# Optimization experiments

Hardware: AMD Instinct MI355X
Metric: run time of the kernel (lower is better)

The kernel has to match this reference:

```python
import jax, jax.numpy as jnp
import numpy as np

B, S, D = 2, 1024, 1024
NH, DQK, DH = 8, 64, 128
CAP = 15.0
EPS = 1e-6


def setup_inputs() -> dict:
    key = jax.random.key(0)
    ks = jax.random.split(key, 8)
    s = 0.02
    return {
        "x": jax.random.normal(ks[0], (B, S, D), jnp.float32),
        "Wq": jax.random.normal(ks[1], (D, NH * DQK), jnp.float32) * s,
        "Wk": jax.random.normal(ks[2], (D, NH * DQK), jnp.float32) * s,
        "Wv": jax.random.normal(ks[3], (D, NH * DH), jnp.float32) * s,
        "Wi": jax.random.normal(ks[4], (D, NH), jnp.float32) * s,
        "bi": jnp.zeros((NH,), jnp.float32),
        "Wf": jax.random.normal(ks[5], (D, NH), jnp.float32) * s,
        "bf": jnp.ones((NH,), jnp.float32),
        "Wog": jax.random.normal(ks[6], (D, D), jnp.float32) * s,
        "ln_w": jnp.ones((NH, DH), jnp.float32),
        "ln_b": jnp.zeros((NH, DH), jnp.float32),
        "Wout": jax.random.normal(ks[7], (NH * DH, D), jnp.float32) * s,
    }


def _mlstm_scan(q, k, v, i, f):
    # q,k: [S,B,NH,DQK]; v: [S,B,NH,DH]; i,f: [S,B,NH]
    b, nh, dqk, dh = q.shape[1], q.shape[2], q.shape[3], v.shape[3]
    scale = dqk ** -0.5
    c0 = jnp.zeros((b, nh, dqk, dh), jnp.float32)
    m0 = jnp.zeros((b, nh), jnp.float32)

    def step(carry, inp):
        c, m = carry
        qt, kt, vt, it, ft = inp
        flog = jax.nn.log_sigmoid(ft)
        m_new = jnp.maximum(flog + m, it)
        f_act = jnp.exp(flog + m - m_new)
        i_act = jnp.exp(it - m_new)
        kv = jnp.einsum('bhi,bhj->bhij', kt, vt)
        c_new = f_act[..., None, None] * c + i_act[..., None, None] * kv
        ht = jnp.einsum('bhij,bhi->bhj', c_new, qt * scale)
        return (c_new, m_new), ht

    _, h = jax.lax.scan(step, (c0, m0), (q, k, v, i, f))
    return h  # [S,B,NH,DH]


def reference(x, Wq, Wk, Wv, Wi, bi, Wf, bf, Wog, ln_w, ln_b, Wout):
    b, s, d = x.shape
    nh, dh = ln_w.shape
    dqk = Wq.shape[1] // nh
    # projections -> time-major [S,B,NH,*]
    q = (x @ Wq).reshape(b, s, nh, dqk).transpose(1, 0, 2, 3)
    k = (x @ Wk).reshape(b, s, nh, dqk).transpose(1, 0, 2, 3)
    v = (x @ Wv).reshape(b, s, nh, dh).transpose(1, 0, 2, 3)
    i = (x @ Wi + bi).transpose(1, 0, 2)
    f = (x @ Wf + bf).transpose(1, 0, 2)
    h = _mlstm_scan(q, k, v, i, f)           # [S,B,NH,DH]
    h = h.transpose(1, 2, 0, 3)              # [B,NH,S,DH]
    # per-head layernorm (unbiased=False variance)
    mean = h.mean(-1, keepdims=True)
    var = ((h - mean) ** 2).mean(-1, keepdims=True)
    hn = (h - mean) / jnp.sqrt(var + EPS)
    hn = hn * ln_w[None, :, None, :] + ln_b[None, :, None, :]
    hn = hn.transpose(0, 2, 1, 3).reshape(b, s, nh * dh)  # [B,S,v_dim]
    o = jax.nn.sigmoid(jnp.tanh((x @ Wog) / CAP) * CAP)
    return (hn * o) @ Wout
```

## Files before the change

### kernel.cpp

```cpp
#include <hip/hip_runtime.h>
#include <math.h>

#define NB_B   2
#define NB_S   1024
#define NB_D   1024
#define NB_NH  8
#define NB_DQK 64
#define NB_DH  128
#define NCH    8
#define CL     128

typedef __attribute__((ext_vector_type(8))) short  short8v;
typedef __attribute__((ext_vector_type(4))) float  f32x4;
typedef __attribute__((ext_vector_type(8))) unsigned short ushort8v;
typedef __attribute__((ext_vector_type(4))) unsigned short ushort4v;

__device__ __forceinline__ unsigned short f2bf(float f) {
  unsigned u = __float_as_uint(f);
  unsigned r = (u + 0x7FFFu + ((u >> 16) & 1u)) >> 16;
  return (unsigned short)r;
}
__device__ __forceinline__ float bf2f(unsigned short h) {
  return __uint_as_float(((unsigned)h) << 16);
}

#define GLD_LDS16(g, l) __builtin_amdgcn_global_load_lds( \
    (const __attribute__((address_space(1))) void*)(g),   \
    (__attribute__((address_space(3))) void*)(l), 16, 0, 0)

#define MFMA_BF16(a, b, c) __builtin_amdgcn_mfma_f32_16x16x32_bf16((a), (b), (c), 0, 0, 0)

constexpr size_t BF(size_t elems) { return elems / 2; }
constexpr size_t SZ_QK1 = BF(2048ull * 512);
constexpr size_t SZ_PVX = BF(2048ull * 2048);
constexpr size_t SZ_XH  = BF(2048ull * 1024);
constexpr size_t SZ_XL  = BF(2048ull * 1024);
constexpr size_t SZ_WHI = BF(3072ull * 1024);
constexpr size_t SZ_WLO = BF(1024ull * 1024);
constexpr size_t SZ_WTO = BF(1024ull * 1024);
constexpr size_t SZ_GBUF= 16ull * 1024;
constexpr size_t SZ_DL  = 16ull * 8 * 8192;
constexpr size_t SZ_HNG = BF(2048ull * 1024);

constexpr size_t OFF_QH  = 0;
constexpr size_t OFF_QL  = OFF_QH  + SZ_QK1;
constexpr size_t OFF_KH  = OFF_QL  + SZ_QK1;
constexpr size_t OFF_KL  = OFF_KH  + SZ_QK1;
constexpr size_t OFF_PVX = OFF_KL  + SZ_QK1;
constexpr size_t OFF_XH  = OFF_PVX + SZ_PVX;
constexpr size_t OFF_XL  = OFF_XH  + SZ_XH;
constexpr size_t OFF_WHI = OFF_XL  + SZ_XL;
constexpr size_t OFF_WLO = OFF_WHI + SZ_WHI;
constexpr size_t OFF_WTO = OFF_WLO + SZ_WLO;
constexpr size_t OFF_IV  = OFF_WTO + SZ_WTO;
constexpr size_t OFF_FV  = OFF_IV  + SZ_GBUF;
constexpr size_t OFF_G   = OFF_FV  + SZ_GBUF;
constexpr size_t OFF_GM  = OFF_G   + SZ_GBUF;
constexpr size_t OFF_DL  = OFF_GM  + SZ_GBUF;
constexpr size_t OFF_HNG = OFF_DL  + SZ_DL;
constexpr size_t WS_TOTAL = OFF_HNG + SZ_HNG;
static_assert(OFF_PVX == 2097152, "Qh+Ql+Kh+Kl must equal old Pqk footprint");
static_assert(SZ_QK1 == 524288, "each qk plane is 2048x512 bf16 = 524,288 float slots");

__device__ __forceinline__ void transp_body(
    const float* __restrict__ src,
    unsigned short* __restrict__ hi, unsigned short* __restrict__ lo,
    int N, int nt, int kt, int tid, float (*Ls)[65])
{
  #pragma unroll
  for (int p = 0; p < 16; ++p) {
    int lin = p * 256 + tid;
    int kr = lin >> 6, nc = lin & 63;
    Ls[kr][nc] = src[(size_t)(kt*64 + kr) * N + nt*64 + nc];
  }
  __syncthreads();
  #pragma unroll
  for (int p = 0; p < 16; ++p) {
    int lin = p * 256 + tid;
    int nr = lin >> 6, kc = lin & 63;
    float v = Ls[kc][nr];
    unsigned short h = f2bf(v);
    size_t di = (size_t)(nt*64 + nr) * 1024 + kt*64 + kc;
    hi[di] = h;
    if (lo) lo[di] = f2bf(v - bf2f(h));
  }
}

__global__ __launch_bounds__(256) void prep(
    const float* __restrict__ x,
    const float* __restrict__ Wi, const float* __restrict__ bi,
    const float* __restrict__ Wf, const float* __restrict__ bf,
    const float* __restrict__ Wq, const float* __restrict__ Wk,
    const float* __restrict__ Wv, const float* __restrict__ Wog,
    const float* __restrict__ Wout,
    unsigned short* __restrict__ xh, unsigned short* __restrict__ xl,
    float* __restrict__ iv, float* __restrict__ fv,
    unsigned short* __restrict__ Whi, unsigned short* __restrict__ Wlo,
    unsigned short* __restrict__ WtO)
{
  __shared__ float Ls[64][65];
  const int bx = blockIdx.x, tid = threadIdx.x;
  if (bx < 512) {
    const int row = bx * 4 + (tid >> 6);
    const int l = tid & 63;
    const float4* xr4 = (const float4*)(x + (size_t)row * NB_D);
    float ai[8] = {}, af[8] = {};
    #pragma unroll
    for (int p = 0; p < 4; ++p) {
      int q4i = l + p * 64;
      float4 xv = xr4[q4i];
      int k0 = q4i * 4;
      const float* xs = (const float*)&xv;
      ushort4v h4, l4;
      #pragma unroll
      for (int j = 0; j < 4; ++j) {
        float xsv = xs[j];
        unsigned short hh = f2bf(xsv);
        h4[j] = hh; l4[j] = f2bf(xsv - bf2f(hh));
        const float4* wi4 = (const float4*)(Wi + (size_t)(k0 + j) * 8);
        const float4* wf4 = (const float4*)(Wf + (size_t)(k0 + j) * 8);
        float4 w0 = wi4[0], w1 = wi4[1];
        float4 v0 = wf4[0], v1 = wf4[1];
        ai[0] += xsv*w0.x; ai[1] += xsv*w0.y; ai[2] += xsv*w0.z; ai[3] += xsv*w0.w;
        ai[4] += xsv*w1.x; ai[5] += xsv*w1.y; ai[6] += xsv*w1.z; ai[7] += xsv*w1.w;
        af[0] += xsv*v0.x; af[1] += xsv*v0.y; af[2] += xsv*v0.z; af[3] += xsv*v0.w;
        af[4] += xsv*v1.x; af[5] += xsv*v1.y; af[6] += xsv*v1.z; af[7] += xsv*v1.w;
      }
      *(ushort4v*)(xh + (size_t)row * NB_D + k0) = h4;
      *(ushort4v*)(xl + (size_t)row * NB_D + k0) = l4;
    }
    #pragma unroll
    for (int off = 1; off < 64; off <<= 1) {
      #pragma unroll
      for (int cc = 0; cc < 8; ++cc) {
        ai[cc] += __shfl_xor(ai[cc], off);
        af[cc] += __shfl_xor(af[cc], off);
      }
    }
    if (l == 0) {
      int b = row >> 10, s = row & (NB_S - 1);
      #pragma unroll
      for (int cc = 0; cc < 8; ++cc) {
        iv[(size_t)(b*NB_NH + cc) * NB_S + s] = ai[cc] + bi[cc];
        fv[(size_t)(b*NB_NH + cc) * NB_S + s] = af[cc] + bf[cc];
      }
    }
  } else {
    const int idx = bx - 512;
    const int xq = idx & 63, kt = idx >> 6;
    if (xq < 8)       transp_body(Wq,   Whi,              Wlo,            512,  xq,      kt, tid, Ls);
    else if (xq < 16) transp_body(Wk,   Whi +  512*1024,  Wlo + 512*1024, 512,  xq - 8,  kt, tid, Ls);
    else if (xq < 32) transp_body(Wv,   Whi + 1024*1024,  nullptr,        1024, xq - 16, kt, tid, Ls);
    else if (xq < 48) transp_body(Wog,  Whi + 2048*1024,  nullptr,        1024, xq - 32, kt, tid, Ls);
    else              transp_body(Wout, WtO,              nullptr,        1024, xq - 48, kt, tid, Ls);
  }
}

__global__ __launch_bounds__(256) void gemm_proj(
    const unsigned short* __restrict__ xh,
    const unsigned short* __restrict__ xl,
    const unsigned short* __restrict__ Whi,
    const unsigned short* __restrict__ Wlo,
    unsigned short* __restrict__ Qh, unsigned short* __restrict__ Ql,
    unsigned short* __restrict__ Kh, unsigned short* __restrict__ Kl,
    unsigned short* __restrict__ Pvx,
    const float* __restrict__ iv, const float* __restrict__ fv,
    float* __restrict__ gv, float* __restrict__ Gv)
{
  __shared__ __align__(16) char smem[49152];
  const int tid  = threadIdx.x;

  if (blockIdx.x < 16) {
    if (tid >= 64) return;
    const int bh = blockIdx.x, l = tid;
    const int base = bh * NB_S + l * 16;
    float fl[16];
    float run = 0.f;
    #pragma unroll
    for (int u = 0; u < 16; ++u) {
      float fr = fv[base + u];
      float flog = (fr >= 0.f) ? -log1pf(expf(-fr)) : (fr - log1pf(expf(fr)));
      run += flog; fl[u] = run;
    }
    float tot = run, sc = tot;
    #pragma unroll
    for (int off = 1; off < 64; off <<= 1) {
      float t = __shfl_up(sc, off);
      if (l >= off) sc += t;
    }
    float excl = sc - tot;
    float gm[16]; float rmax = -1e30f;
    #pragma unroll
    for (int u = 0; u < 16; ++u) {
      float bt = excl + fl[u];
      float g = iv[base + u] - bt;
      gv[base + u] = g;
      rmax = fmaxf(rmax, g); gm[u] = rmax;
    }
    float mx = rmax;
    #pragma unroll
    for (int off = 1; off < 64; off <<= 1) {
      float t = __shfl_up(mx, off);
      if (l >= off) mx = fmaxf(mx, t);
    }
    float em = __shfl_up(mx, 1);
    if (l == 0) em = -1e30f;
    #pragma unroll
    for (int u = 0; u < 16; ++u)
      Gv[base + u] = fmaxf(0.f, fmaxf(em, gm[u]));
    return;
  }

  const int gx   = blockIdx.x - 16;
  const int bid  = ((gx & 7) << 6) | (gx >> 3);
  const int wid  = tid >> 6, lane = tid & 63;
  const int wm   = wid >> 1, wn = wid & 1;
  const int lrow = lane & 15;
  const int lk   = (lane >> 4) * 16;
  const int srow = tid >> 3;
  const int scb  = (tid & 7) << 4;
  const int ldsW = wid * 1024;

  if (!(bid & 1)) {
    const int h  = bid >> 1;
    const int ct = h & 7, bm = h >> 3;
    char* Ah = smem;
    char* Al = smem + 8192;
    char* Bh = smem + 16384;
    char* Bl = smem + 32768;
    const char* xhB = (const char*)xh;
    const char* xlB = (const char*)xl;
    const char* whB = (const char*)(Whi + (size_t)ct*128*1024);
    const char* wlB = (const char*)(Wlo + (size_t)ct*128*1024);

    size_t gA[2], gB[4];
    #pragma unroll
    for (int i = 0; i < 2; ++i) {
      int row = i * 32 + srow;
      int cbs = scb ^ ((row & 7) << 4);
      gA[i] = (size_t)(bm*64 + row) * 2048 + cbs;
    }
    #pragma unroll
    for (int i = 0; i < 4; ++i) {
      int row = i * 32 + srow;
      int cbs = scb ^ ((row & 7) << 4);
      gB[i] = (size_t)row * 2048 + cbs;
    }

    f32x4 acc[2][4];
    const f32x4 z4 = { 0.f, 0.f, 0.f, 0.f };
    #pragma unroll
    for (int m = 0; m < 2; ++m)
      #pragma unroll
      for (int n = 0; n < 4; ++n) acc[m][n] = z4;

    for (int kt = 0; kt < 16; ++kt) {
      __syncthreads();
      #pragma unroll
      for (int i = 0; i < 2; ++i) GLD_LDS16(xhB + gA[i] + kt*128, Ah + i*4096 + ldsW);
      #pragma unroll
      for (int i = 0; i < 2; ++i) GLD_LDS16(xlB + gA[i] + kt*128, Al + i*4096 + ldsW);
      #pragma unroll
      for (int i = 0; i < 4; ++i) GLD_LDS16(whB + gB[i] + kt*128, Bh + i*4096 + ldsW);
      #pragma unroll
      for (int i = 0; i < 4; ++i) GLD_LDS16(wlB + gB[i] + kt*128, Bl + i*4096 + ldsW);
      __syncthreads();

      #pragma unroll
      for (int kk = 0; kk < 2; ++kk) {
        short8v ah[2], al[2], bh[4], bl[4];
        #pragma unroll
        for (int m = 0; m < 2; ++m) {
          int row = wm*32 + m*16 + lrow;
          int kb  = (kk*64 + lk) ^ ((row & 7) << 4);
          ah[m] = *(const short8v*)(Ah + row*128 + kb);
          al[m] = *(const short8v*)(Al + row*128 + kb);
        }
        #pragma unroll
        for (int n = 0; n < 4; ++n) {
          int row = wn*64 + n*16 + lrow;
          int kb  = (kk*64 + lk) ^ ((row & 7) << 4);
          bh[n] = *(const short8v*)(Bh + row*128 + kb);
          bl[n] = *(const short8v*)(Bl + row*128 + kb);
        }
        #pragma unroll
        for (int m = 0; m < 2; ++m)
          #pragma unroll
          for (int n = 0; n < 4; ++n) {
            acc[m][n] = MFMA_BF16(ah[m], bh[n], acc[m][n]);
            acc[m][n] = MFMA_BF16(al[m], bh[n], acc[m][n]);
            acc[m][n] = MFMA_BF16(ah[m], bl[n], acc[m][n]);
          }
      }
    }

    const int crow0 = bm*64 + wm*32 + ((lane >> 4) << 2);
    const int ccol0 = (ct & 3)*128 + wn*64 + lrow;
    unsigned short* Hd = (ct < 4) ? Qh : Kh;
    unsigned short* Ld = (ct < 4) ? Ql : Kl;
    #pragma unroll
    for (int m = 0; m < 2; ++m)
      #pragma unroll
      for (int n = 0; n < 4; ++n)
        #pragma unroll
        for (int r = 0; r < 4; ++r) {
          float v = acc[m][n][r];
          unsigned short hh = f2bf(v);
          size_t idx = (size_t)(crow0 + m*16 + r) * 512 + ccol0 + n*16;
          Hd[idx] = hh;
          Ld[idx] = f2bf(v - bf2f(hh));
        }
  } else {
    const int l  = bid >> 1;
    const int ct = l & 15, bm = l >> 4;
    char* As = smem;
    char* Bs = smem + 16384;
    const char* xhB = (const char*)xh;
    const char* wB  = (const char*)(Whi + (size_t)(8 + ct)*128*1024);

    size_t gA[4], gB[4];
    #pragma unroll
    for (int i = 0; i < 4; ++i) {
      int row = i * 32 + srow;
      int cbs = scb ^ ((row & 7) << 4);
      gA[i] = (size_t)(bm*128 + row) * 2048 + cbs;
      gB[i] = (size_t)row * 2048 + cbs;
    }

    f32x4 acc[4][4];
    const f32x4 z4 = { 0.f, 0.f, 0.f, 0.f };
    #pragma unroll
    for (int m = 0; m < 4; ++m)
      #pragma unroll
      for (int n = 0; n < 4; ++n) acc[m][n] = z4;

    for (int kt = 0; kt < 16; ++kt) {
      __syncthreads();
      #pragma unroll
      for (int i = 0; i < 4; ++i) GLD_LDS16(xhB + gA[i] + kt*128, As + i*4096 + ldsW);
      #pragma unroll
      for (int i = 0; i < 4; ++i) GLD_LDS16(wB  + gB[i] + kt*128, Bs + i*4096 + ldsW);
      __syncthreads();

      #pragma unroll
      for (int kk = 0; kk < 2; ++kk) {
        short8v a[4], b[4];
        #pragma unroll
        for (int m = 0; m < 4; ++m) {
          int row = wm*64 + m*16 + lrow;
          int kb  = (kk*64 + lk) ^ ((row & 7) << 4);
          a[m] = *(const short8v*)(As + row*128 + kb);
        }
        #pragma unroll
        for (int n = 0; n < 4; ++n) {
          int row = wn*64 + n*16 + lrow;
          int kb  = (kk*64 + lk) ^ ((row & 7) << 4);
          b[n] = *(const short8v*)(Bs + row*128 + kb);
        }
        #pragma unroll
        for (int m = 0; m < 4; ++m)
          #pragma unroll
          for (int n = 0; n < 4; ++n)
            acc[m][n] = MFMA_BF16(a[m], b[n], acc[m][n]);
      }
    }

    const int crow0 = bm*128 + wm*64 + ((lane >> 4) << 2);
    const int ccol0 = ct*128 + wn*64 + lrow;
    #pragma unroll
    for (int m = 0; m < 4; ++m)
      #pragma unroll
      for (int n = 0; n < 4; ++n)
        #pragma unroll
        for (int r = 0; r < 4; ++r)
          Pvx[(size_t)(crow0 + m*16 + r) * 2048 + ccol0 + n*16] = f2bf(acc[m][n][r]);
  }
}

__global__ __launch_bounds__(256) void gemm_out64(
    const unsigned short* __restrict__ A,
    const unsigned short* __restrict__ Bt,
    float* __restrict__ C, int ldc)
{
  __shared__ __align__(16) unsigned short As[128*64];
  __shared__ __align__(16) unsigned short Bs[64*64];
  const int tid  = threadIdx.x;
  const int bid  = ((blockIdx.x & 7) << 5) | (blockIdx.x >> 3);
  const int cn   = bid & 15, bm = bid >> 4;
  const int wid  = tid >> 6, lane = tid & 63;
  const int wm   = wid >> 1, wn = wid & 1;
  const int lrow = lane & 15;
  const int lk   = (lane >> 4) * 16;

  f32x4 acc[4][2];
  const f32x4 z4 = { 0.f, 0.f, 0.f, 0.f };
  #pragma unroll
  for (int m = 0; m < 4; ++m)
    #pragma unroll
    for (int n = 0; n < 2; ++n) acc[m][n] = z4;

  const int srow = tid >> 3;
  const int scb  = (tid & 7) << 4;
  const char* Ab = (const char*)A;
  const char* Bb = (const char*)Bt;
  size_t gA[4], gB[2];
  #pragma unroll
  for (int i = 0; i < 4; ++i) {
    int row = i * 32 + srow;
    int cbs = scb ^ ((row & 7) << 4);
    gA[i] = (size_t)(bm*128 + row) * 2048 + cbs;
  }
  #pragma unroll
  for (int i = 0; i < 2; ++i) {
    int row = i * 32 + srow;
    int cbs = scb ^ ((row & 7) << 4);
    gB[i] = (size_t)(cn*64 + row) * 2048 + cbs;
  }
  const int ldsW = wid * 1024;

  for (int kt = 0; kt < 16; ++kt) {
    __syncthreads();
    #pragma unroll
    for (int i = 0; i < 4; ++i)
      GLD_LDS16(Ab + gA[i] + kt*128, (char*)As + i*4096 + ldsW);
    #pragma unroll
    for (int i = 0; i < 2; ++i)
      GLD_LDS16(Bb + gB[i] + kt*128, (char*)Bs + i*4096 + ldsW);
    __syncthreads();

    #pragma unroll
    for (int kk = 0; kk < 2; ++kk) {
      short8v a[4], b[2];
      #pragma unroll
      for (int m = 0; m < 4; ++m) {
        int row = wm*64 + m*16 + lrow;
        int kb  = (kk*64 + lk) ^ ((row & 7) << 4);
        a[m] = *(const short8v*)((const char*)As + row*128 + kb);
      }
      #pragma unroll
      for (int n = 0; n < 2; ++n) {
        int row = wn*32 + n*16 + lrow;
        int kb  = (kk*64 + lk) ^ ((row & 7) << 4);
        b[n] = *(const short8v*)((const char*)Bs + row*128 + kb);
      }
      #pragma unroll
      for (int m = 0; m < 4; ++m)
        #pragma unroll
        for (int n = 0; n < 2; ++n)
          acc[m][n] = MFMA_BF16(a[m], b[n], acc[m][n]);
    }
  }

  const int crow0 = bm*128 + wm*64 + ((lane >> 4) << 2);
  const int ccol0 = cn*64 + wn*32 + (lane & 15);
  #pragma unroll
  for (int m = 0; m < 4; ++m)
    #pragma unroll
    for (int n = 0; n < 2; ++n)
      #pragma unroll
      for (int r = 0; r < 4; ++r)
        C[(size_t)(crow0 + m*16 + r) * ldc + ccol0 + n*16] = acc[m][n][r];
}

__global__ __launch_bounds__(128) void chunk_local(
    const unsigned short* __restrict__ Kh, const unsigned short* __restrict__ Pvx,
    const float* __restrict__ gv, const float* __restrict__ Gv,
    float* __restrict__ Dloc)
{
  __shared__ float ks[16][68];
  __shared__ float vs[16][68];
  __shared__ float wsg[16];
  const int bx = ((blockIdx.x & 7) << 5) | (blockIdx.x >> 3);
  const int bh = bx >> 4, c = (bx >> 1) & 7, jh = bx & 1;
  const int b = bh >> 3, h = bh & 7;
  const int tid = threadIdx.x;
  const int rg = tid >> 3, cg = tid & 7;
  const int i0 = rg * 4;
  float acc[4][8] = {};
  const float Gend = Gv[bh*NB_S + c*CL + CL - 1];
  const unsigned short* kbp = Kh + ((size_t)b*NB_S + c*CL) * 512 + h*NB_DQK;
  const unsigned short* vbp = Pvx + ((size_t)b*NB_S + c*CL) * 2048 + h*NB_DH + jh*64;
  const float* gbp = gv + bh*NB_S + c*CL;
  for (int sb = 0; sb < 8; ++sb) {
    __syncthreads();
    #pragma unroll
    for (int p = 0; p < 2; ++p) {
      int qd = tid + p*128; int r = qd >> 4, cq = qd & 15;
      ushort4v k4 = *(const ushort4v*)(kbp + (size_t)(sb*16 + r)*512 + cq*4);
      ks[r][cq*4+0] = bf2f(k4[0]); ks[r][cq*4+1] = bf2f(k4[1]);
      ks[r][cq*4+2] = bf2f(k4[2]); ks[r][cq*4+3] = bf2f(k4[3]);
    }
    #pragma unroll
    for (int p = 0; p < 2; ++p) {
      int qd = tid + p*128; int r = qd >> 4, cq = qd & 15;
      ushort4v v4 = *(const ushort4v*)(vbp + (size_t)(sb*16 + r)*2048 + cq*4);
      vs[r][cq*4+0] = bf2f(v4[0]); vs[r][cq*4+1] = bf2f(v4[1]);
      vs[r][cq*4+2] = bf2f(v4[2]); vs[r][cq*4+3] = bf2f(v4[3]);
    }
    if (tid < 16) wsg[tid] = expf(gbp[sb*16 + tid] - Gend);
    __syncthreads();
    #pragma unroll
    for (int s = 0; s < 16; ++s) {
      float w = wsg[s];
      float4 kq = *(const float4*)(&ks[s][i0]);
      float wk[4] = { w*kq.x, w*kq.y, w*kq.z, w*kq.w };
      #pragma unroll
      for (int m = 0; m < 2; ++m) {
        float4 vq = *(const float4*)(&vs[s][cg*4 + m*32]);
        #pragma unroll
        for (int u = 0; u < 4; ++u) {
          acc[u][m*4+0] += wk[u]*vq.x;
          acc[u][m*4+1] += wk[u]*vq.y;
          acc[u][m*4+2] += wk[u]*vq.z;
          acc[u][m*4+3] += wk[u]*vq.w;
        }
      }
    }
  }
  float* dst = Dloc + ((size_t)bh*NCH + c) * (NB_DQK*NB_DH) + jh*64;
  #pragma unroll
  for (int u = 0; u < 4; ++u)
    #pragma unroll
    for (int m = 0; m < 2; ++m) {
      float4 o4 = { acc[u][m*4+0], acc[u][m*4+1], acc[u][m*4+2], acc[u][m*4+3] };
      *(float4*)(dst + (size_t)(i0+u)*NB_DH + cg*4 + m*32) = o4;
    }
}

__global__ __launch_bounds__(256,1) void chunk_out(
    const unsigned short* __restrict__ Qh, const unsigned short* __restrict__ Ql,
    const unsigned short* __restrict__ Kh, const unsigned short* __restrict__ Kl,
    const unsigned short* __restrict__ Pvx,
    const float* __restrict__ gv, const float* __restrict__ Gv,
    const float* __restrict__ Dloc,
    const float* __restrict__ lnw, const float* __restrict__ lnb,
    unsigned short* __restrict__ hng)
{
  __shared__ __align__(16) char smem[131072];
  __shared__ float gsh[128], Gsh[128], rsh[128];
  constexpr int QHo = 0, QLo = 8192, KHo = 16384, KLo = 32768;
  constexpr int ATT = 49152, VT = 65536, CBH = 98304, CBL = 114688;

  const int bx = ((blockIdx.x & 7) << 5) | (blockIdx.x >> 3);
  const int half = bx & 1, c = (bx >> 1) & 7, bh = bx >> 4;
  const int b = bh >> 3, h = bh & 7;
  const int tid = threadIdx.x;
  const int wid = tid >> 6, lane = tid & 63;
  const int lrow = lane & 15;
  const int lkB  = (lane >> 4) * 16;
  const size_t rowbase = (size_t)b*NB_S + (size_t)c*CL;
  const int sgbase = bh*NB_S + c*CL;
  const int ldsW = wid * 1024;

  {
    const int srow8 = tid >> 3;
    const int scb8  = (tid & 7) << 4;
    const char* QhB = (const char*)Qh;
    const char* QlB = (const char*)Ql;
    const char* KhB = (const char*)Kh;
    const char* KlB = (const char*)Kl;
    #pragma unroll
    for (int i = 0; i < 2; ++i) {
      int r = i*32 + srow8;
      size_t off = (size_t)(rowbase + half*64 + r)*1024 + h*128 + (scb8 ^ ((r & 7) << 4));
      GLD_LDS16(QhB + off, smem + QHo + i*4096 + ldsW);
      GLD_LDS16(QlB + off, smem + QLo + i*4096 + ldsW);
    }
    #pragma unroll
    for (int i = 0; i < 4; ++i) {
      int r = i*32 + srow8;
      size_t off = (size_t)(rowbase + r)*1024 + h*128 + (scb8 ^ ((r & 7) << 4));
      GLD_LDS16(KhB + off, smem + KHo + i*4096 + ldsW);
      GLD_LDS16(KlB + off, smem + KLo + i*4096 + ldsW);
    }
  }

  if (tid < 128) {
    float gval = gv[sgbase + tid];
    float Gval = Gv[sgbase + tid];
    gsh[tid] = gval; Gsh[tid] = Gval;
    float Gprev = (c > 0) ? Gv[sgbase - 1] : 0.f;
    rsh[tid] = 0.125f * expf(Gprev - Gval);
  }

  #pragma unroll
  for (int p = 0; p < 8; ++p) {
    int lin = p*256 + tid;
    int s = lin >> 4, j0 = (lin & 15) * 8;
    ushort8v v8 = *(const ushort8v*)(Pvx + (rowbase + s)*2048 + h*NB_DH + j0);
    #pragma unroll
    for (int j = 0; j < 8; ++j) {
      int jj = j0 + j;
      int off = (jj*256 + s*2) ^ ((jj & 7) << 4);
      *(unsigned short*)(smem + VT + off) = v8[j];
    }
  }
  {
    float4 cbacc[8];
    #pragma unroll
    for (int p = 0; p < 8; ++p) cbacc[p] = float4{0.f,0.f,0.f,0.f};
    const float Gcm1 = (c > 0) ? Gv[sgbase - 1] : 0.f;
    for (int cp = 0; cp < c; ++cp) {
      float wgt = expf(Gv[bh*NB_S + cp*CL + CL - 1] - Gcm1);
      const float4* dl4 = (const float4*)(Dloc + ((size_t)bh*NCH + cp)*8192);
      #pragma unroll
      for (int p = 0; p < 8; ++p) {
        float4 d = dl4[p*256 + tid];
        cbacc[p].x += wgt*d.x; cbacc[p].y += wgt*d.y;
        cbacc[p].z += wgt*d.z; cbacc[p].w += wgt*d.w;
      }
    }
    #pragma unroll
    for (int p = 0; p < 8; ++p) {
      int lin = p*256 + tid;
      int i = lin >> 5, j0 = (lin & 31) * 4;
      float vv[4] = { cbacc[p].x, cbacc[p].y, cbacc[p].z, cbacc[p].w };
      #pragma unroll
      for (int w = 0; w < 4; ++w) {
        int jj = j0 + w;
        int off = (jj*128 + i*2) ^ ((jj & 7) << 4);
        unsigned short hh = f2bf(vv[w]);
        *(unsigned short*)(smem + CBH + off) = hh;
        *(unsigned short*)(smem + CBL + off) = f2bf(vv[w] - bf2f(hh));
      }
    }
  }
  __syncthreads();

  const f32x4 z4 = { 0.f, 0.f, 0.f, 0.f };
  const int trow = wid*16 + lrow;

  f32x4 sacc[8];
  #pragma unroll
  for (int n = 0; n < 8; ++n) sacc[n] = z4;
  #pragma unroll
  for (int kk = 0; kk < 2; ++kk) {
    int qb = kk*64 + lkB;
    int ab = (trow*128 + qb) ^ ((trow & 7) << 4);
    short8v aqh = *(const short8v*)(smem + QHo + ab);
    short8v aql = *(const short8v*)(smem + QLo + ab);
    #pragma unroll
    for (int n = 0; n < 8; ++n) {
      int srw = n*16 + lrow;
      int bb = (srw*128 + qb) ^ ((srw & 7) << 4);
      short8v bkh = *(const short8v*)(smem + KHo + bb);
      short8v bkl = *(const short8v*)(smem + KLo + bb);
      sacc[n] = MFMA_BF16(aqh, bkh, sacc[n]);
      sacc[n] = MFMA_BF16(aql, bkh, sacc[n]);
      sacc[n] = MFMA_BF16(aqh, bkl, sacc[n]);
    }
  }
  {
    int td[4]; float gt[4];
    #pragma unroll
    for (int r = 0; r < 4; ++r) {
      td[r] = wid*16 + ((lane >> 4) << 2) + r;
      gt[r] = Gsh[half*64 + td[r]];
    }
    #pragma unroll
    for (int n = 0; n < 8; ++n) {
      int s = n*16 + lrow;
      float gs = gsh[s];
      #pragma unroll
      for (int r = 0; r < 4; ++r) {
        float w = 0.125f * expf(gs - gt[r]);
        float val = (s <= half*64 + td[r]) ? sacc[n][r]*w : 0.f;
        int off = (td[r]*256 + s*2) ^ ((td[r] & 7) << 4);
        *(unsigned short*)(smem + ATT + off) = f2bf(val);
      }
    }
  }

  f32x4 h2[8];
  #pragma unroll
  for (int n = 0; n < 8; ++n) h2[n] = z4;
  #pragma unroll
  for (int kk = 0; kk < 2; ++kk) {
    int qb = kk*64 + lkB;
    int ab = (trow*128 + qb) ^ ((trow & 7) << 4);
    short8v aqh = *(const short8v*)(smem + QHo + ab);
    short8v aql = *(const short8v*)(smem + QLo + ab);
    #pragma unroll
    for (int n = 0; n < 8; ++n) {
      int jrw = n*16 + lrow;
      int bb = (jrw*128 + qb) ^ ((jrw & 7) << 4);
      short8v bch = *(const short8v*)(smem + CBH + bb);
      short8v bcl = *(const short8v*)(smem + CBL + bb);
      h2[n] = MFMA_BF16(aqh, bch, h2[n]);
      h2[n] = MFMA_BF16(aql, bch, h2[n]);
      h2[n] = MFMA_BF16(aqh, bcl, h2[n]);
    }
  }
  __syncthreads();

  f32x4 h1[8];
  #pragma unroll
  for (int n = 0; n < 8; ++n) h1[n] = z4;
  #pragma unroll
  for (int kk = 0; kk < 4; ++kk) {
    int ab = (trow*256 + kk*64 + lkB) ^ ((trow & 7) << 4);
    short8v aat = *(const short8v*)(smem + ATT + ab);
    #pragma unroll
    for (int n = 0; n < 8; ++n) {
      int jrw = n*16 + lrow;
      int bb = (jrw*256 + kk*64 + lkB) ^ ((jrw & 7) << 4);
      short8v bvt = *(const short8v*)(smem + VT + bb);
      h1[n] = MFMA_BF16(aat, bvt, h1[n]);
    }
  }
  __syncthreads();

  float* Hb = (float*)smem;
  {
    #pragma unroll
    for (int r = 0; r < 4; ++r) {
      int tl = wid*16 + ((lane >> 4) << 2) + r;
      float rr = rsh[half*64 + tl];
      #pragma unroll
      for (int n = 0; n < 8; ++n)
        Hb[tl*132 + n*16 + lrow] = h1[n][r] + rr*h2[n][r];
    }
  }
  __syncthreads();

  const int tr = tid >> 4, tc = tid & 15;
  float lw[8], lb[8];
  {
    float4 a0 = *(const float4*)(lnw + h*NB_DH + tc*4);
    float4 a1 = *(const float4*)(lnw + h*NB_DH + tc*4 + 64);
    lw[0]=a0.x; lw[1]=a0.y; lw[2]=a0.z; lw[3]=a0.w;
    lw[4]=a1.x; lw[5]=a1.y; lw[6]=a1.z; lw[7]=a1.w;
    float4 b0 = *(const float4*)(lnb + h*NB_DH + tc*4);
    float4 b1 = *(const float4*)(lnb + h*NB_DH + tc*4 + 64);
    lb[0]=b0.x; lb[1]=b0.y; lb[2]=b0.z; lb[3]=b0.w;
    lb[4]=b1.x; lb[5]=b1.y; lb[6]=b1.z; lb[7]=b1.w;
  }
  #pragma unroll
  for (int u = 0; u < 4; ++u) {
    int tl = tr*4 + u;
    int t  = half*64 + tl;
    float hrow[8];
    float4 hl0 = *(const float4*)(&Hb[tl*132 + tc*4]);
    float4 hl1 = *(const float4*)(&Hb[tl*132 + tc*4 + 64]);
    hrow[0]=hl0.x; hrow[1]=hl0.y; hrow[2]=hl0.z; hrow[3]=hl0.w;
    hrow[4]=hl1.x; hrow[5]=hl1.y; hrow[6]=hl1.z; hrow[7]=hl1.w;
    float sum = 0.f, ssq = 0.f;
    #pragma unroll
    for (int x = 0; x < 8; ++x) { sum += hrow[x]; ssq += hrow[x]*hrow[x]; }
    #pragma unroll
    for (int off = 1; off < 16; off <<= 1) {
      sum += __shfl_xor(sum, off);
      ssq += __shfl_xor(ssq, off);
    }
    float mean = sum * (1.f/NB_DH);
    float var  = ssq * (1.f/NB_DH) - mean*mean;
    float rstd = rsqrtf(var + 1e-6f);
    #pragma unroll
    for (int m = 0; m < 2; ++m) {
      ushort4v xo4 = *(const ushort4v*)(Pvx + (rowbase + t)*2048 + 1024 + h*NB_DH + tc*4 + m*64);
      float xov[4] = { bf2f(xo4[0]), bf2f(xo4[1]), bf2f(xo4[2]), bf2f(xo4[3]) };
      unsigned short res[4];
      #pragma unroll
      for (int w = 0; w < 4; ++w) {
        int x = m*4 + w;
        float hn = (hrow[x] - mean)*rstd*lw[x] + lb[x];
        float tt = tanhf(xov[w]*(1.f/15.f))*15.f;
        float o = 1.f/(1.f + expf(-tt));
        res[w] = f2bf(hn*o);
      }
      ushort4v r4 = { res[0], res[1], res[2], res[3] };
      *(ushort4v*)(hng + (rowbase + t)*1024 + h*NB_DH + tc*4 + m*64) = r4;
    }
  }
}

extern "C" void kernel_launch(void* const* d_in, const int* in_sizes, int n_in,
                              void* d_out, int out_size, void* d_ws, size_t ws_size,
                              hipStream_t stream)
{
  (void)in_sizes; (void)n_in; (void)out_size; (void)ws_size;
  const float* x   = (const float*)d_in[0];
  const float* Wq  = (const float*)d_in[1];
  const float* Wk  = (const float*)d_in[2];
  const float* Wv  = (const float*)d_in[3];
  const float* Wi  = (const float*)d_in[4];
  const float* bi  = (const float*)d_in[5];
  const float* Wf  = (const float*)d_in[6];
  const float* bf  = (const float*)d_in[7];
  const float* Wog = (const float*)d_in[8];
  const float* lnw = (const float*)d_in[9];
  const float* lnb = (const float*)d_in[10];
  const float* Wout= (const float*)d_in[11];
  float* out = (float*)d_out;
  float* ws  = (float*)d_ws;

  unsigned short* Qh  = (unsigned short*)(ws + OFF_QH);
  unsigned short* Ql  = (unsigned short*)(ws + OFF_QL);
  unsigned short* Kh  = (unsigned short*)(ws + OFF_KH);
  unsigned short* Kl  = (unsigned short*)(ws + OFF_KL);
  unsigned short* Pvx = (unsigned short*)(ws + OFF_PVX);
  unsigned short* xh  = (unsigned short*)(ws + OFF_XH);
  unsigned short* xl  = (unsigned short*)(ws + OFF_XL);
  unsigned short* Whi = (unsigned short*)(ws + OFF_WHI);
  unsigned short* Wlo = (unsigned short*)(ws + OFF_WLO);
  unsigned short* WtO = (unsigned short*)(ws + OFF_WTO);
  float*          iv  = ws + OFF_IV;
  float*          fv  = ws + OFF_FV;
  float*          g   = ws + OFF_G;
  float*          G   = ws + OFF_GM;
  float*          Dl  = ws + OFF_DL;
  unsigned short* hng = (unsigned short*)(ws + OFF_HNG);

  prep     <<<1536, 256, 0, stream>>>(x, Wi, bi, Wf, bf, Wq, Wk, Wv, Wog, Wout,
                                      xh, xl, iv, fv, Whi, Wlo, WtO);

  gemm_proj<<<528, 256, 0, stream>>>(xh, xl, Whi, Wlo, Qh, Ql, Kh, Kl, Pvx,
                                     iv, fv, g, G);

  chunk_local<<<256, 128, 0, stream>>>(Kh, Pvx, g, G, Dl);
  chunk_out  <<<256, 256, 0, stream>>>(Qh, Ql, Kh, Kl, Pvx, g, G, Dl, lnw, lnb, hng);

  gemm_out64 <<<256, 256, 0, stream>>>(hng, WtO, out, 1024);
}
```

Before: 109.0 us.

## Fuse chunk_local and chunk_out into one cooperative kernel with grid sync

The per-chunk KV state computation now runs as the first phase of the chunk output kernel, using 256 threads per block and the existing shared memory. A grid-wide cooperative sync separates it from the output phase, and the kernel is launched with hipLaunchCooperativeKernel. The aim is to drop one kernel launch and its inter-kernel gap. In exchange it adds a grid barrier and requires all 256 blocks to be co-resident, which launch_bounds(256,1) and the 128KB+ shared memory allow on a 256-CU device.

```diff
diff --git a/kernel.cpp b/kernel.cpp
--- a/kernel.cpp
+++ b/kernel.cpp
@@ -1,5 +1,8 @@
 #include <hip/hip_runtime.h>
+#include <hip/hip_cooperative_groups.h>
 #include <math.h>
+
+namespace cg = cooperative_groups;
 
 #define NB_B   2
 #define NB_S   1024
@@ -462,77 +465,12 @@
         C[(size_t)(crow0 + m*16 + r) * ldc + ccol0 + n*16] = acc[m][n][r];
 }
 
-__global__ __launch_bounds__(128) void chunk_local(
-    const unsigned short* __restrict__ Kh, const unsigned short* __restrict__ Pvx,
-    const float* __restrict__ gv, const float* __restrict__ Gv,
-    float* __restrict__ Dloc)
-{
-  __shared__ float ks[16][68];
-  __shared__ float vs[16][68];
-  __shared__ float wsg[16];
-  const int bx = ((blockIdx.x & 7) << 5) | (blockIdx.x >> 3);
-  const int bh = bx >> 4, c = (bx >> 1) & 7, jh = bx & 1;
-  const int b = bh >> 3, h = bh & 7;
-  const int tid = threadIdx.x;
-  const int rg = tid >> 3, cg = tid & 7;
-  const int i0 = rg * 4;
-  float acc[4][8] = {};
-  const float Gend = Gv[bh*NB_S + c*CL + CL - 1];
-  const unsigned short* kbp = Kh + ((size_t)b*NB_S + c*CL) * 512 + h*NB_DQK;
-  const unsigned short* vbp = Pvx + ((size_t)b*NB_S + c*CL) * 2048 + h*NB_DH + jh*64;
-  const float* gbp = gv + bh*NB_S + c*CL;
-  for (int sb = 0; sb < 8; ++sb) {
-    __syncthreads();
-    #pragma unroll
-    for (int p = 0; p < 2; ++p) {
-      int qd = tid + p*128; int r = qd >> 4, cq = qd & 15;
-      ushort4v k4 = *(const ushort4v*)(kbp + (size_t)(sb*16 + r)*512 + cq*4);
-      ks[r][cq*4+0] = bf2f(k4[0]); ks[r][cq*4+1] = bf2f(k4[1]);
-      ks[r][cq*4+2] = bf2f(k4[2]); ks[r][cq*4+3] = bf2f(k4[3]);
-    }
-    #pragma unroll
-    for (int p = 0; p < 2; ++p) {
-      int qd = tid + p*128; int r = qd >> 4, cq = qd & 15;
-      ushort4v v4 = *(const ushort4v*)(vbp + (size_t)(sb*16 + r)*2048 + cq*4);
-      vs[r][cq*4+0] = bf2f(v4[0]); vs[r][cq*4+1] = bf2f(v4[1]);
-      vs[r][cq*4+2] = bf2f(v4[2]); vs[r][cq*4+3] = bf2f(v4[3]);
-    }
-    if (tid < 16) wsg[tid] = expf(gbp[sb*16 + tid] - Gend);
-    __syncthreads();
-    #pragma unroll
-    for (int s = 0; s < 16; ++s) {
-      float w = wsg[s];
-      float4 kq = *(const float4*)(&ks[s][i0]);
-      float wk[4] = { w*kq.x, w*kq.y, w*kq.z, w*kq.w };
-      #pragma unroll
-      for (int m = 0; m < 2; ++m) {
-        float4 vq = *(const float4*)(&vs[s][cg*4 + m*32]);
-        #pragma unroll
-        for (int u = 0; u < 4; ++u) {
-          acc[u][m*4+0] += wk[u]*vq.x;
-          acc[u][m*4+1] += wk[u]*vq.y;
-          acc[u][m*4+2] += wk[u]*vq.z;
-          acc[u][m*4+3] += wk[u]*vq.w;
-        }
-      }
-    }
-  }
-  float* dst = Dloc + ((size_t)bh*NCH + c) * (NB_DQK*NB_DH) + jh*64;
-  #pragma unroll
-  for (int u = 0; u < 4; ++u)
-    #pragma unroll
-    for (int m = 0; m < 2; ++m) {
-      float4 o4 = { acc[u][m*4+0], acc[u][m*4+1], acc[u][m*4+2], acc[u][m*4+3] };
-      *(float4*)(dst + (size_t)(i0+u)*NB_DH + cg*4 + m*32) = o4;
-    }
-}
-
-__global__ __launch_bounds__(256,1) void chunk_out(
+__global__ __launch_bounds__(256,1) void tail_fused(
     const unsigned short* __restrict__ Qh, const unsigned short* __restrict__ Ql,
     const unsigned short* __restrict__ Kh, const unsigned short* __restrict__ Kl,
     const unsigned short* __restrict__ Pvx,
     const float* __restrict__ gv, const float* __restrict__ Gv,
-    const float* __restrict__ Dloc,
+    float* __restrict__ Dloc,
     const float* __restrict__ lnw, const float* __restrict__ lnb,
     unsigned short* __restrict__ hng)
 {
@@ -541,10 +479,62 @@
   constexpr int QHo = 0, QLo = 8192, KHo = 16384, KLo = 32768;
   constexpr int ATT = 49152, VT = 65536, CBH = 98304, CBL = 114688;
 
+  const int tid = threadIdx.x;
   const int bx = ((blockIdx.x & 7) << 5) | (blockIdx.x >> 3);
+
+  {
+    const int bhA = bx >> 4, cA = (bx >> 1) & 7, jh = bx & 1;
+    const int bA = bhA >> 3, hA = bhA & 7;
+    float* ks = (float*)smem;
+    float* vs = (float*)(smem + 8192);
+    float* wsg = (float*)(smem + 16384);
+    const int rg = tid >> 4, cgi = tid & 15;
+    const int i0 = rg * 4;
+    float accA[4][4] = {};
+    const float Gend = Gv[bhA*NB_S + cA*CL + CL - 1];
+    const unsigned short* kbp = Kh + ((size_t)bA*NB_S + cA*CL) * 512 + hA*NB_DQK;
+    const unsigned short* vbp = Pvx + ((size_t)bA*NB_S + cA*CL) * 2048 + hA*NB_DH + jh*64;
+    const float* gbp = gv + bhA*NB_S + cA*CL;
+    for (int sb = 0; sb < 8; ++sb) {
+      __syncthreads();
+      {
+        int r = tid >> 4, cq = tid & 15;
+        ushort4v k4 = *(const ushort4v*)(kbp + (size_t)(sb*16 + r)*512 + cq*4);
+        ks[r*68 + cq*4+0] = bf2f(k4[0]); ks[r*68 + cq*4+1] = bf2f(k4[1]);
+        ks[r*68 + cq*4+2] = bf2f(k4[2]); ks[r*68 + cq*4+3] = bf2f(k4[3]);
+        ushort4v v4 = *(const ushort4v*)(vbp + (size_t)(sb*16 + r)*2048 + cq*4);
+        vs[r*68 + cq*4+0] = bf2f(v4[0]); vs[r*68 + cq*4+1] = bf2f(v4[1]);
+        vs[r*68 + cq*4+2] = bf2f(v4[2]); vs[r*68 + cq*4+3] = bf2f(v4[3]);
+      }
+      if (tid < 16) wsg[tid] = expf(gbp[sb*16 + tid] - Gend);
+      __syncthreads();
+      #pragma unroll
+      for (int s = 0; s < 16; ++s) {
+        float w = wsg[s];
+        float4 kq = *(const float4*)(&ks[s*68 + i0]);
+        float wk[4] = { w*kq.x, w*kq.y, w*kq.z, w*kq.w };
+        float4 vq = *(const float4*)(&vs[s*68 + cgi*4]);
+        #pragma unroll
+        for (int u = 0; u < 4; ++u) {
+          accA[u][0] += wk[u]*vq.x;
+          accA[u][1] += wk[u]*vq.y;
+          accA[u][2] += wk[u]*vq.z;
+          accA[u][3] += wk[u]*vq.w;
+        }
+      }
+    }
+    float* dst = Dloc + ((size_t)bhA*NCH + cA) * (NB_DQK*NB_DH) + jh*64;
+    #pragma unroll
+    for (int u = 0; u < 4; ++u) {
+      float4 o4 = { accA[u][0], accA[u][1], accA[u][2], accA[u][3] };
+      *(float4*)(dst + (size_t)(i0+u)*NB_DH + cgi*4) = o4;
+    }
+  }
+
+  cg::this_grid().sync();
+
   const int half = bx & 1, c = (bx >> 1) & 7, bh = bx >> 4;
   const int b = bh >> 3, h = bh & 7;
-  const int tid = threadIdx.x;
   const int wid = tid >> 6, lane = tid & 63;
   const int lrow = lane & 15;
   const int lkB  = (lane >> 4) * 16;
@@ -817,8 +807,13 @@
   gemm_proj<<<528, 256, 0, stream>>>(xh, xl, Whi, Wlo, Qh, Ql, Kh, Kl, Pvx,
                                      iv, fv, g, G);
 
-  chunk_local<<<256, 128, 0, stream>>>(Kh, Pvx, g, G, Dl);
-  chunk_out  <<<256, 256, 0, stream>>>(Qh, Ql, Kh, Kl, Pvx, g, G, Dl, lnw, lnb, hng);
+  {
+    void* args[] = { (void*)&Qh, (void*)&Ql, (void*)&Kh, (void*)&Kl, (void*)&Pvx,
+                     (void*)&g, (void*)&G, (void*)&Dl,
+                     (void*)&lnw, (void*)&lnb, (void*)&hng };
+    hipLaunchCooperativeKernel((const void*)tail_fused, dim3(256), dim3(256),
+                               args, 0, stream);
+  }
 
   gemm_out64 <<<256, 256, 0, stream>>>(hng, WtO, out, 1024);
 }
```

Result: slower. 142.5 us (+30.7%).
